# Optimization experiments

Hardware: AMD Instinct MI355X
Metric: run time of the kernel (lower is better)

Reference implementation:

```python
import jax, jax.numpy as jnp
import numpy as np

D_MODEL = 1024
HEADS = 16
DIM_HEAD = 64
INNER = HEADS * DIM_HEAD


def setup_inputs() -> dict:
    key = jax.random.key(0)
    ks = jax.random.split(key, 5)
    B, N = 4, 2048
    x = jax.random.normal(ks[0], (B, N, D_MODEL), dtype=jnp.float32)
    w_qkv = jax.random.normal(ks[1], (INNER * 3, D_MODEL), dtype=jnp.float32) * (1.0 / np.sqrt(D_MODEL))
    b_qkv = jax.random.normal(ks[2], (INNER * 3,), dtype=jnp.float32) * 0.02
    w_out = jax.random.normal(ks[3], (D_MODEL, INNER), dtype=jnp.float32) * (1.0 / np.sqrt(INNER))
    logit_scale = jnp.log(10.0 * jnp.ones((HEADS, 1, 1), dtype=jnp.float32))
    return {"x": x, "w_qkv": w_qkv, "b_qkv": b_qkv, "w_out": w_out, "logit_scale": logit_scale}


def _l2norm(t, eps=1e-12):
    # matches F.normalize(dim=-1): x / max(||x||, eps)
    n = jnp.sqrt(jnp.sum(t * t, axis=-1, keepdims=True))
    return t / jnp.maximum(n, eps)


def reference(x, w_qkv, b_qkv, w_out, logit_scale):
    B, N, C = x.shape
    qkv = x @ w_qkv.T + b_qkv                      # [B,N,3*INNER]
    qkv = qkv.reshape(B, N, 3, HEADS, DIM_HEAD)
    qkv = jnp.transpose(qkv, (2, 0, 3, 1, 4))       # [3,B,H,N,Dh]
    q, k, v = qkv[0], qkv[1], qkv[2]
    attn = jnp.einsum('bhnd,bhmd->bhnm', _l2norm(q), _l2norm(k))
    scale = jnp.exp(jnp.minimum(logit_scale, jnp.log(1.0 / 0.01)))  # [H,1,1]
    attn = attn * scale[None]                       # broadcast over batch
    attn = jax.nn.softmax(attn, axis=-1)
    out = jnp.einsum('bhnm,bhmd->bhnd', attn, v)    # [B,H,N,Dh]
    out = jnp.transpose(out, (0, 2, 1, 3)).reshape(B, N, C)
    return out @ w_out.T
```

## Files before the change

### kernel.cpp

```cpp
#include <hip/hip_runtime.h>

typedef __attribute__((ext_vector_type(8))) __bf16 bf16x8;
typedef __attribute__((ext_vector_type(4))) float f32x4;
typedef unsigned short u16;

__device__ __forceinline__ u16 f2bf(float f) {
    union { float f; unsigned u; } v; v.f = f;
    unsigned r = v.u + 0x7FFFu + ((v.u >> 16) & 1u);
    return (u16)(r >> 16);
}
__device__ __forceinline__ float bf2f(u16 h) {
    union { unsigned u; float f; } v; v.u = ((unsigned)h) << 16;
    return v.f;
}
__device__ __forceinline__ u16 f2bf_n(float f) {
    union { __bf16 b; u16 u; } t; t.b = (__bf16)f; return t.u;
}
__device__ __forceinline__ bf16x8 ld_bf16x8(const u16* p) {
    union { uint4 u; bf16x8 b; } t;
    t.u = *(const uint4*)p;
    return t.b;
}
__device__ __forceinline__ void async16(const void* g, const void* l) {
    __builtin_amdgcn_global_load_lds((const __attribute__((address_space(1))) void*)g,
                                     (__attribute__((address_space(3))) void*)l, 16, 0, 0);
}

#define BATCH 4
#define NSEQ 2048
#define HEADS 16
#define DH 64
#define DMODEL 1024
#define MROWS 8192
#define NQKV 3072

__global__ void split_bf16(const float* __restrict__ src, u16* __restrict__ hi,
                           u16* __restrict__ lo, int n) {
    int i = blockIdx.x * blockDim.x + threadIdx.x;
    if (i < n) {
        float f = src[i];
        u16 h = f2bf(f);
        hi[i] = h;
        lo[i] = f2bf(f - bf2f(h));
    }
}
__global__ void cvt_bf16(const float* __restrict__ src, u16* __restrict__ dst, int n) {
    int i = blockIdx.x * blockDim.x + threadIdx.x;
    if (i < n) dst[i] = f2bf(src[i]);
}

__global__ __launch_bounds__(256) void qkv_gemm(
    const u16* __restrict__ A,
    const u16* __restrict__ Bh, const u16* __restrict__ Bl,
    const float* __restrict__ bias,
    u16* __restrict__ Qn, u16* __restrict__ Kn, u16* __restrict__ Vt) {
    const int K = DMODEL, TK = 32;
    __shared__ __align__(16) u16 sA[128 * 32];
    __shared__ __align__(16) u16 sBh[128 * 32], sBl[128 * 32];
    const int tid = threadIdx.x, wave = tid >> 6, lane = tid & 63;
    const int quad = lane >> 4, l16 = lane & 15;
    const int m0 = blockIdx.x * 128, n0 = blockIdx.y * 128;
    const int wm = (wave & 1) * 64, wn = (wave >> 1) * 64;
    f32x4 acc[4][4] = {};

    for (int k0 = 0; k0 < K; k0 += TK) {
        __syncthreads();
        #pragma unroll
        for (int pass = 0; pass < 2; ++pass) {
            const int c = pass * 256 + tid;
            const int row = c >> 2, part = c & 3;
            const int ldsOff = (pass * 256 + wave * 64) * 16;
            const size_t ga = (size_t)(m0 + row) * K + k0 + part * 8;
            const size_t gb = (size_t)(n0 + row) * K + k0 + part * 8;
            async16(A + ga, (const char*)sA + ldsOff);
            async16(Bh + gb, (const char*)sBh + ldsOff);
            async16(Bl + gb, (const char*)sBl + ldsOff);
        }
        __syncthreads();
        bf16x8 a[4];
        #pragma unroll
        for (int mt = 0; mt < 4; ++mt)
            a[mt] = ld_bf16x8(&sA[(wm + mt * 16 + l16) * TK + quad * 8]);
        #pragma unroll
        for (int nt = 0; nt < 4; ++nt) {
            const int cix = wn + nt * 16 + l16;
            bf16x8 bh = ld_bf16x8(&sBh[cix * TK + quad * 8]);
            bf16x8 bl = ld_bf16x8(&sBl[cix * TK + quad * 8]);
            #pragma unroll
            for (int mt = 0; mt < 4; ++mt) {
                acc[mt][nt] = __builtin_amdgcn_mfma_f32_16x16x32_bf16(a[mt], bh, acc[mt][nt], 0, 0, 0);
                acc[mt][nt] = __builtin_amdgcn_mfma_f32_16x16x32_bf16(a[mt], bl, acc[mt][nt], 0, 0, 0);
            }
        }
    }

    #pragma unroll
    for (int nt = 0; nt < 4; ++nt) {
        const float bv = bias[n0 + wn + nt * 16 + l16];
        #pragma unroll
        for (int mt = 0; mt < 4; ++mt)
            #pragma unroll
            for (int r = 0; r < 4; ++r)
                acc[mt][nt][r] += bv;
    }

    if (n0 < 2048) {
        u16* dst = (n0 < 1024) ? Qn : Kn;
        const int nq = (n0 & 1023) + wn;
        const int hh = nq >> 6;
        #pragma unroll
        for (int mt = 0; mt < 4; ++mt) {
            float ss[4] = {};
            #pragma unroll
            for (int nt = 0; nt < 4; ++nt)
                #pragma unroll
                for (int r = 0; r < 4; ++r)
                    ss[r] += acc[mt][nt][r] * acc[mt][nt][r];
            #pragma unroll
            for (int r = 0; r < 4; ++r) {
                ss[r] += __shfl_xor(ss[r], 1);
                ss[r] += __shfl_xor(ss[r], 2);
                ss[r] += __shfl_xor(ss[r], 4);
                ss[r] += __shfl_xor(ss[r], 8);
                ss[r] = 1.f / fmaxf(sqrtf(ss[r]), 1e-12f);
            }
            const int mbase = m0 + wm + mt * 16 + quad * 4;
            const int b = mbase >> 11, n = mbase & 2047;
            #pragma unroll
            for (int r = 0; r < 4; ++r) {
                size_t rowoff = (((size_t)(b * HEADS + hh)) * NSEQ + n + r) * DH;
                #pragma unroll
                for (int nt = 0; nt < 4; ++nt)
                    dst[rowoff + nt * 16 + l16] = f2bf_n(acc[mt][nt][r] * ss[r]);
            }
        }
    } else {
        const int nv = (n0 - 2048) + wn;
        const int hh = nv >> 6;
        #pragma unroll
        for (int nt = 0; nt < 4; ++nt) {
            const int d = nt * 16 + l16;
            #pragma unroll
            for (int mt = 0; mt < 4; ++mt) {
                const int mbase = m0 + wm + mt * 16 + quad * 4;
                const int b = mbase >> 11, n = mbase & 2047;
                ushort4 t;
                t.x = f2bf_n(acc[mt][nt][0]);
                t.y = f2bf_n(acc[mt][nt][1]);
                t.z = f2bf_n(acc[mt][nt][2]);
                t.w = f2bf_n(acc[mt][nt][3]);
                *(ushort4*)&Vt[(((size_t)(b * HEADS + hh)) * DH + d) * NSEQ + n] = t;
            }
        }
    }
}

__global__ __launch_bounds__(256) void out_gemm(
    const u16* __restrict__ A, const u16* __restrict__ B, float* __restrict__ C) {
    const int K = DMODEL, N = DMODEL, TK = 32;
    __shared__ __align__(16) u16 sA[128 * 32], sB[128 * 32];
    const int tid = threadIdx.x, wave = tid >> 6, lane = tid & 63;
    const int quad = lane >> 4, l16 = lane & 15;
    const int m0 = blockIdx.x * 128, n0 = blockIdx.y * 128;
    const int wm = (wave & 1) * 64, wn = (wave >> 1) * 64;
    f32x4 acc[4][4] = {};

    for (int k0 = 0; k0 < K; k0 += TK) {
        __syncthreads();
        #pragma unroll
        for (int pass = 0; pass < 2; ++pass) {
            const int c = pass * 256 + tid;
            const int row = c >> 2, part = c & 3;
            const int ldsOff = (pass * 256 + wave * 64) * 16;
            const size_t ga = (size_t)(m0 + row) * K + k0 + part * 8;
            const size_t gb = (size_t)(n0 + row) * K + k0 + part * 8;
            async16(A + ga, (const char*)sA + ldsOff);
            async16(B + gb, (const char*)sB + ldsOff);
        }
        __syncthreads();
        bf16x8 a[4];
        #pragma unroll
        for (int mt = 0; mt < 4; ++mt)
            a[mt] = ld_bf16x8(&sA[(wm + mt * 16 + l16) * TK + quad * 8]);
        #pragma unroll
        for (int nt = 0; nt < 4; ++nt) {
            bf16x8 b = ld_bf16x8(&sB[(wn + nt * 16 + l16) * TK + quad * 8]);
            #pragma unroll
            for (int mt = 0; mt < 4; ++mt)
                acc[mt][nt] = __builtin_amdgcn_mfma_f32_16x16x32_bf16(a[mt], b, acc[mt][nt], 0, 0, 0);
        }
    }
    #pragma unroll
    for (int nt = 0; nt < 4; ++nt) {
        const int n = n0 + wn + nt * 16 + l16;
        #pragma unroll
        for (int mt = 0; mt < 4; ++mt) {
            const int mbase = m0 + wm + mt * 16 + quad * 4;
            #pragma unroll
            for (int r = 0; r < 4; ++r)
                C[(size_t)(mbase + r) * N + n] = acc[mt][nt][r];
        }
    }
}

__global__ __launch_bounds__(512) void flash_attn(
    const u16* __restrict__ Q, const u16* __restrict__ Kn, const u16* __restrict__ Vt,
    const float* __restrict__ lsc, u16* __restrict__ AO) {
    const int bh = blockIdx.x;
    const int q0 = blockIdx.y * 128;
    const int h = bh & (HEADS - 1), b = bh >> 4;
    const int tid = threadIdx.x, wave = tid >> 6, lane = tid & 63;
    const int quad = lane >> 4, l16 = lane & 15;
    const float scale = __expf(fminf(lsc[h], 4.6051702f));
    const float c1 = scale * 1.4426950408889634f;

    __shared__ __align__(16) u16 Ks[64][72];
    __shared__ __align__(16) u16 Vs[64][72];
    __shared__ __align__(16) u16 Ps[8][16][72];

    const u16* qbase = Q + ((size_t)bh * NSEQ + q0 + wave * 16) * DH;
    bf16x8 qa[2];
    qa[0] = ld_bf16x8(qbase + l16 * DH + quad * 8);
    qa[1] = ld_bf16x8(qbase + l16 * DH + 32 + quad * 8);

    f32x4 O[4] = {};
    float lr[4] = {0.f, 0.f, 0.f, 0.f};

    const int row = tid >> 3, part = tid & 7;
    const u16* kb = Kn + (size_t)bh * NSEQ * DH + (size_t)row * DH + part * 8;
    const u16* vb = Vt + (size_t)bh * DH * NSEQ + (size_t)row * NSEQ + part * 8;

    uint4 kA = *(const uint4*)kb;
    uint4 vA = *(const uint4*)vb;
    uint4 kB, vB;

    auto compute = [&]() {
        f32x4 S[4] = {};
        __builtin_amdgcn_s_setprio(1);
        #pragma unroll
        for (int nt = 0; nt < 4; ++nt) {
            bf16x8 k0 = ld_bf16x8(&Ks[nt * 16 + l16][quad * 8]);
            bf16x8 k1 = ld_bf16x8(&Ks[nt * 16 + l16][32 + quad * 8]);
            S[nt] = __builtin_amdgcn_mfma_f32_16x16x32_bf16(qa[0], k0, S[nt], 0, 0, 0);
            S[nt] = __builtin_amdgcn_mfma_f32_16x16x32_bf16(qa[1], k1, S[nt], 0, 0, 0);
        }
        __builtin_amdgcn_s_setprio(0);

        #pragma unroll
        for (int nt = 0; nt < 4; ++nt) {
            #pragma unroll
            for (int r = 0; r < 4; ++r) {
                float pv = __builtin_amdgcn_exp2f(__builtin_fmaf(S[nt][r], c1, -c1));
                lr[r] += pv;
                Ps[wave][quad * 4 + r][nt * 16 + l16] = f2bf_n(pv);
            }
        }
        asm volatile("s_waitcnt lgkmcnt(0)" ::: "memory");
        bf16x8 pa0 = ld_bf16x8(&Ps[wave][l16][quad * 8]);
        bf16x8 pa1 = ld_bf16x8(&Ps[wave][l16][32 + quad * 8]);

        __builtin_amdgcn_s_setprio(1);
        #pragma unroll
        for (int dt = 0; dt < 4; ++dt) {
            bf16x8 v0 = ld_bf16x8(&Vs[dt * 16 + l16][quad * 8]);
            bf16x8 v1 = ld_bf16x8(&Vs[dt * 16 + l16][32 + quad * 8]);
            O[dt] = __builtin_amdgcn_mfma_f32_16x16x32_bf16(pa0, v0, O[dt], 0, 0, 0);
            O[dt] = __builtin_amdgcn_mfma_f32_16x16x32_bf16(pa1, v1, O[dt], 0, 0, 0);
        }
        __builtin_amdgcn_s_setprio(0);
    };

    #pragma unroll 1
    for (int kt = 0; kt < NSEQ; kt += 128) {
        asm volatile("s_waitcnt lgkmcnt(0)" ::: "memory");
        __builtin_amdgcn_s_barrier();
        kB = *(const uint4*)(kb + (size_t)(kt + 64) * DH);
        vB = *(const uint4*)(vb + (kt + 64));
        asm volatile("s_waitcnt vmcnt(2)" ::: "memory");
        *(uint4*)&Ks[row][part * 8] = kA;
        *(uint4*)&Vs[row][part * 8] = vA;
        asm volatile("s_waitcnt lgkmcnt(0)" ::: "memory");
        __builtin_amdgcn_s_barrier();
        compute();

        asm volatile("s_waitcnt lgkmcnt(0)" ::: "memory");
        __builtin_amdgcn_s_barrier();
        {
            const int nk = (kt + 128) < NSEQ ? (kt + 128) : 0;
            kA = *(const uint4*)(kb + (size_t)nk * DH);
            vA = *(const uint4*)(vb + nk);
        }
        asm volatile("s_waitcnt vmcnt(2)" ::: "memory");
        *(uint4*)&Ks[row][part * 8] = kB;
        *(uint4*)&Vs[row][part * 8] = vB;
        asm volatile("s_waitcnt lgkmcnt(0)" ::: "memory");
        __builtin_amdgcn_s_barrier();
        compute();
    }

    #pragma unroll
    for (int r = 0; r < 4; ++r) {
        float s = lr[r];
        s += __shfl_xor(s, 1);
        s += __shfl_xor(s, 2);
        s += __shfl_xor(s, 4);
        s += __shfl_xor(s, 8);
        lr[r] = fmaxf(s, 1e-30f);
    }

    #pragma unroll
    for (int r = 0; r < 4; ++r) {
        float inv = 1.f / lr[r];
        size_t orow = (size_t)b * NSEQ + q0 + wave * 16 + quad * 4 + r;
        #pragma unroll
        for (int dt = 0; dt < 4; ++dt)
            AO[orow * DMODEL + h * DH + dt * 16 + l16] = f2bf_n(O[dt][r] * inv);
    }
}

extern "C" void kernel_launch(void* const* d_in, const int* in_sizes, int n_in,
                              void* d_out, int out_size, void* d_ws, size_t ws_size,
                              hipStream_t stream) {
    const float* x    = (const float*)d_in[0];
    const float* wqkv = (const float*)d_in[1];
    const float* bqkv = (const float*)d_in[2];
    const float* wout = (const float*)d_in[3];
    const float* lsc  = (const float*)d_in[4];

    char* ws = (char*)d_ws;
    u16* xb   = (u16*)(ws + 0);
    u16* wqh  = (u16*)(ws + 16777216);
    u16* wql  = (u16*)(ws + 23068672);
    u16* wob  = (u16*)(ws + 29360128);
    u16* qn   = (u16*)(ws + 31457280);
    u16* kn   = (u16*)(ws + 48234496);
    u16* vt   = (u16*)(ws + 65011712);
    u16* ao   = xb;

    cvt_bf16<<<MROWS * DMODEL / 256, 256, 0, stream>>>(x, xb, MROWS * DMODEL);
    split_bf16<<<NQKV * DMODEL / 256, 256, 0, stream>>>(wqkv, wqh, wql, NQKV * DMODEL);
    cvt_bf16<<<DMODEL * DMODEL / 256, 256, 0, stream>>>(wout, wob, DMODEL * DMODEL);

    qkv_gemm<<<dim3(MROWS / 128, NQKV / 128), 256, 0, stream>>>(xb, wqh, wql, bqkv, qn, kn, vt);
    flash_attn<<<dim3(BATCH * HEADS, NSEQ / 128), 512, 0, stream>>>(qn, kn, vt, lsc, ao);
    out_gemm<<<dim3(MROWS / 128, DMODEL / 128), 256, 0, stream>>>(ao, wob, (float*)d_out);
}
```

Before: 357.9 us.

## Triple-buffer QKV GEMM with swizzled LDS, larger tiles and 512 threads

Rewrites the QKV projection GEMM as a 3-stage async LDS pipeline over 64 K-steps, with hi and lo weight halves streamed as separate passes rather than interleaved per step. The block tile grows to 256x128 with 8 waves, LDS reads use an XOR swizzle to avoid bank conflicts, and MFMA sections run at raised priority. The aim is to hide global-load latency and drop one of the two barriers per step. In exchange it uses more LDS per block, and the output epilogue must still match the new wave-to-tile mapping.

```diff
diff --git a/kernel.cpp b/kernel.cpp
--- a/kernel.cpp
+++ b/kernel.cpp
@@ -49,50 +49,72 @@
     if (i < n) dst[i] = f2bf(src[i]);
 }
 
-__global__ __launch_bounds__(256) void qkv_gemm(
+#define QBUF 24576
+
+__global__ __launch_bounds__(512, 2) void qkv_gemm(
     const u16* __restrict__ A,
     const u16* __restrict__ Bh, const u16* __restrict__ Bl,
     const float* __restrict__ bias,
     u16* __restrict__ Qn, u16* __restrict__ Kn, u16* __restrict__ Vt) {
-    const int K = DMODEL, TK = 32;
-    __shared__ __align__(16) u16 sA[128 * 32];
-    __shared__ __align__(16) u16 sBh[128 * 32], sBl[128 * 32];
+    __shared__ __align__(1024) char lds[3 * QBUF];
     const int tid = threadIdx.x, wave = tid >> 6, lane = tid & 63;
     const int quad = lane >> 4, l16 = lane & 15;
-    const int m0 = blockIdx.x * 128, n0 = blockIdx.y * 128;
-    const int wm = (wave & 1) * 64, wn = (wave >> 1) * 64;
+    const int wr = wave >> 1, wc = wave & 1;
+    const int wm = wr * 64, wn = wc * 64;
+    const int m0 = blockIdx.x * 256, n0 = blockIdx.y * 128;
+
+    const int srow = tid >> 2;
+    const int sq = (tid & 3) ^ ((srow >> 1) & 3);
+    const char* aSrc0 = (const char*)A + (size_t)(m0 + srow) * 2048 + sq * 16;
+    const char* aSrc1 = aSrc0 + (size_t)128 * 2048;
+    const size_t bRow = (size_t)(n0 + srow) * 2048 + (size_t)(sq * 16);
+    const char* bSrcH = (const char*)Bh + bRow;
+    const char* bSrcL = (const char*)Bl + bRow;
+    const int ldsW = wave * 1024;
+
+    auto stage = [&](int src, int buf) {
+        const int kk = (src & 31) * 64;
+        const char* bs = (src < 32 ? bSrcH : bSrcL) + kk;
+        char* d = lds + buf * QBUF;
+        async16(aSrc0 + kk, d + ldsW);
+        async16(aSrc1 + kk, d + 8192 + ldsW);
+        async16(bs, d + 16384 + ldsW);
+    };
+
+    const int rq = (quad ^ ((l16 >> 1) & 3)) * 16;
+
     f32x4 acc[4][4] = {};
 
-    for (int k0 = 0; k0 < K; k0 += TK) {
-        __syncthreads();
-        #pragma unroll
-        for (int pass = 0; pass < 2; ++pass) {
-            const int c = pass * 256 + tid;
-            const int row = c >> 2, part = c & 3;
-            const int ldsOff = (pass * 256 + wave * 64) * 16;
-            const size_t ga = (size_t)(m0 + row) * K + k0 + part * 8;
-            const size_t gb = (size_t)(n0 + row) * K + k0 + part * 8;
-            async16(A + ga, (const char*)sA + ldsOff);
-            async16(Bh + gb, (const char*)sBh + ldsOff);
-            async16(Bl + gb, (const char*)sBl + ldsOff);
-        }
-        __syncthreads();
-        bf16x8 a[4];
+    stage(0, 0);
+    stage(1, 1);
+
+    int bufc = 0, bufs = 2;
+    #pragma unroll 1
+    for (int t = 0; t < 64; ++t) {
+        asm volatile("s_waitcnt vmcnt(3)" ::: "memory");
+        __builtin_amdgcn_s_barrier();
+        __builtin_amdgcn_sched_barrier(0);
+        stage((t + 2) & 63, bufs);
+        const char* bufA = lds + bufc * QBUF;
+        const char* bufB = bufA + 16384;
+        bf16x8 af[4], bfr[4];
         #pragma unroll
         for (int mt = 0; mt < 4; ++mt)
-            a[mt] = ld_bf16x8(&sA[(wm + mt * 16 + l16) * TK + quad * 8]);
-        #pragma unroll
-        for (int nt = 0; nt < 4; ++nt) {
-            const int cix = wn + nt * 16 + l16;
-            bf16x8 bh = ld_bf16x8(&sBh[cix * TK + quad * 8]);
-            bf16x8 bl = ld_bf16x8(&sBl[cix * TK + quad * 8]);
-            #pragma unroll
-            for (int mt = 0; mt < 4; ++mt) {
-                acc[mt][nt] = __builtin_amdgcn_mfma_f32_16x16x32_bf16(a[mt], bh, acc[mt][nt], 0, 0, 0);
-                acc[mt][nt] = __builtin_amdgcn_mfma_f32_16x16x32_bf16(a[mt], bl, acc[mt][nt], 0, 0, 0);
-            }
-        }
-    }
+            af[mt] = ld_bf16x8((const u16*)(bufA + (wm + mt * 16 + l16) * 64 + rq));
+        #pragma unroll
+        for (int nt = 0; nt < 4; ++nt)
+            bfr[nt] = ld_bf16x8((const u16*)(bufB + (wn + nt * 16 + l16) * 64 + rq));
+        __builtin_amdgcn_s_setprio(1);
+        #pragma unroll
+        for (int nt = 0; nt < 4; ++nt)
+            #pragma unroll
+            for (int mt = 0; mt < 4; ++mt)
+                acc[mt][nt] = __builtin_amdgcn_mfma_f32_16x16x32_bf16(af[mt], bfr[nt], acc[mt][nt], 0, 0, 0);
+        __builtin_amdgcn_s_setprio(0);
+        bufc = (bufc == 2) ? 0 : bufc + 1;
+        bufs = (bufs == 2) ? 0 : bufs + 1;
+    }
+    asm volatile("s_waitcnt vmcnt(0)" ::: "memory");
 
     #pragma unroll
     for (int nt = 0; nt < 4; ++nt) {
@@ -341,7 +363,7 @@
     split_bf16<<<NQKV * DMODEL / 256, 256, 0, stream>>>(wqkv, wqh, wql, NQKV * DMODEL);
     cvt_bf16<<<DMODEL * DMODEL / 256, 256, 0, stream>>>(wout, wob, DMODEL * DMODEL);
 
-    qkv_gemm<<<dim3(MROWS / 128, NQKV / 128), 256, 0, stream>>>(xb, wqh, wql, bqkv, qn, kn, vt);
+    qkv_gemm<<<dim3(MROWS / 256, NQKV / 128), 512, 0, stream>>>(xb, wqh, wql, bqkv, qn, kn, vt);
     flash_attn<<<dim3(BATCH * HEADS, NSEQ / 128), 512, 0, stream>>>(qn, kn, vt, lsc, ao);
     out_gemm<<<dim3(MROWS / 128, DMODEL / 128), 256, 0, stream>>>(ao, wob, (float*)d_out);
 }
```

Result: slower. 382.0 us (+6.8%).

## Rewrite QKV GEMM as 256x256 tiled, double-buffered, swizzled-LDS pipelined kernel

Applied to the files above, without the earlier changes.

Replaces the 128x128 QKV GEMM with a 256x256 tile over 8 waves. It double-buffers 64 KB LDS stages with XOR-swizzled layouts and interleaves async global-to-LDS loads with MFMA phases, using explicit barriers, vmcnt waits and s_setprio. The bf16 hi/lo weight halves are now concatenated along K (32 k-steps) rather than issuing two MFMAs per A fragment. The aim is to hide load latency, cut LDS bank conflicts and raise data reuse per tile, at the cost of heavier register pressure and lower occupancy, plus fragile hand-managed synchronization.

```diff
diff --git a/kernel.cpp b/kernel.cpp
--- a/kernel.cpp
+++ b/kernel.cpp
@@ -49,73 +49,129 @@
     if (i < n) dst[i] = f2bf(src[i]);
 }
 
-__global__ __launch_bounds__(256) void qkv_gemm(
+#define QK_BUF 65536
+
+#define QBAR() asm volatile("s_barrier" ::: "memory")
+
+#define RD_AF(QH, BB) { \
+    _Pragma("unroll") for (int mi = 0; mi < 4; ++mi) { \
+        const int rr = wm + (QH) * 64 + mi * 16 + l16; \
+        af[mi][0] = ld_bf16x8((const u16*)(lds + (BB) + rr * 128 + qsw0)); \
+        af[mi][1] = ld_bf16x8((const u16*)(lds + (BB) + rr * 128 + qsw1)); } }
+
+#define RD_BF(DST, NB, BB) { \
+    _Pragma("unroll") for (int ni = 0; ni < 2; ++ni) { \
+        const int rr = wn + (NB) * 32 + ni * 16 + l16; \
+        DST[ni][0] = ld_bf16x8((const u16*)(lds + (BB) + 32768 + rr * 128 + qsw0)); \
+        DST[ni][1] = ld_bf16x8((const u16*)(lds + (BB) + 32768 + rr * 128 + qsw1)); } }
+
+#define ST_A(KT, H, BB) { \
+    const char* g = aRow + (size_t)(H) * 262144 + (((KT) & 15) << 7); \
+    char* d = lds + (BB) + (H) * 16384 + wave * 1024; \
+    async16(g, d); async16(g + 131072, d + 8192); }
+
+#define ST_B(KT, H, BB) { \
+    const char* g = (((KT) < 16) ? bhRow : blRow) + (size_t)(H) * 262144 + (((KT) & 15) << 7); \
+    char* d = lds + (BB) + 32768 + (H) * 16384 + wave * 1024; \
+    async16(g, d); async16(g + 131072, d + 8192); }
+
+#define MFMA_Q(MIB, NIB) { \
+    __builtin_amdgcn_s_setprio(1); \
+    _Pragma("unroll") for (int ks = 0; ks < 2; ++ks) \
+    _Pragma("unroll") for (int mi = 0; mi < 4; ++mi) \
+    _Pragma("unroll") for (int ni = 0; ni < 2; ++ni) \
+        acc[(MIB) + mi][(NIB) + ni] = __builtin_amdgcn_mfma_f32_16x16x32_bf16( \
+            af[mi][ks], ((NIB) ? b1 : b0)[ni][ks], acc[(MIB) + mi][(NIB) + ni], 0, 0, 0); \
+    __builtin_amdgcn_s_setprio(0); }
+
+__global__ __launch_bounds__(512, 2) void qkv_gemm(
     const u16* __restrict__ A,
     const u16* __restrict__ Bh, const u16* __restrict__ Bl,
     const float* __restrict__ bias,
     u16* __restrict__ Qn, u16* __restrict__ Kn, u16* __restrict__ Vt) {
-    const int K = DMODEL, TK = 32;
-    __shared__ __align__(16) u16 sA[128 * 32];
-    __shared__ __align__(16) u16 sBh[128 * 32], sBl[128 * 32];
+    __shared__ __align__(1024) char lds[2 * QK_BUF];
     const int tid = threadIdx.x, wave = tid >> 6, lane = tid & 63;
     const int quad = lane >> 4, l16 = lane & 15;
-    const int m0 = blockIdx.x * 128, n0 = blockIdx.y * 128;
-    const int wm = (wave & 1) * 64, wn = (wave >> 1) * 64;
-    f32x4 acc[4][4] = {};
-
-    for (int k0 = 0; k0 < K; k0 += TK) {
-        __syncthreads();
-        #pragma unroll
-        for (int pass = 0; pass < 2; ++pass) {
-            const int c = pass * 256 + tid;
-            const int row = c >> 2, part = c & 3;
-            const int ldsOff = (pass * 256 + wave * 64) * 16;
-            const size_t ga = (size_t)(m0 + row) * K + k0 + part * 8;
-            const size_t gb = (size_t)(n0 + row) * K + k0 + part * 8;
-            async16(A + ga, (const char*)sA + ldsOff);
-            async16(Bh + gb, (const char*)sBh + ldsOff);
-            async16(Bl + gb, (const char*)sBl + ldsOff);
-        }
-        __syncthreads();
-        bf16x8 a[4];
-        #pragma unroll
-        for (int mt = 0; mt < 4; ++mt)
-            a[mt] = ld_bf16x8(&sA[(wm + mt * 16 + l16) * TK + quad * 8]);
-        #pragma unroll
-        for (int nt = 0; nt < 4; ++nt) {
-            const int cix = wn + nt * 16 + l16;
-            bf16x8 bh = ld_bf16x8(&sBh[cix * TK + quad * 8]);
-            bf16x8 bl = ld_bf16x8(&sBl[cix * TK + quad * 8]);
-            #pragma unroll
-            for (int mt = 0; mt < 4; ++mt) {
-                acc[mt][nt] = __builtin_amdgcn_mfma_f32_16x16x32_bf16(a[mt], bh, acc[mt][nt], 0, 0, 0);
-                acc[mt][nt] = __builtin_amdgcn_mfma_f32_16x16x32_bf16(a[mt], bl, acc[mt][nt], 0, 0, 0);
-            }
-        }
-    }
+    const int wm = (wave >> 2) * 128, wn = (wave & 3) * 64;
+    const int m0 = blockIdx.x * 256, n0 = blockIdx.y * 256;
+
+    const int lr0 = tid >> 3;
+    const int qs = ((tid & 7) ^ (lr0 & 7)) * 16;
+    const char* aRow  = (const char*)A  + (size_t)(m0 + lr0) * 2048 + qs;
+    const char* bhRow = (const char*)Bh + (size_t)(n0 + lr0) * 2048 + qs;
+    const char* blRow = (const char*)Bl + (size_t)(n0 + lr0) * 2048 + qs;
+
+    const int qsw0 = ((0 * 4 + quad) ^ (l16 & 7)) * 16;
+    const int qsw1 = ((1 * 4 + quad) ^ (l16 & 7)) * 16;
+
+    f32x4 acc[8][4] = {};
+    bf16x8 af[4][2], b0[2][2], b1[2][2];
+
+    ST_A(0, 0, 0); ST_A(0, 1, 0); ST_B(0, 0, 0); ST_B(0, 1, 0);
+    ST_A(1, 0, QK_BUF); ST_A(1, 1, QK_BUF); ST_B(1, 0, QK_BUF); ST_B(1, 1, QK_BUF);
+    asm volatile("s_waitcnt vmcnt(8)" ::: "memory");
+    QBAR();
+
+    #pragma unroll 1
+    for (int t = 0; t < 16; ++t) {
+        const int k1 = 2 * t + 1;
+        const int k2 = (2 * t + 2) & 31;
+        const int k3 = (2 * t + 3) & 31;
+        RD_AF(0, 0); RD_BF(b0, 0, 0);
+        ST_A(k1, 1, QK_BUF);
+        QBAR(); MFMA_Q(0, 0); QBAR();
+
+        RD_BF(b1, 1, 0);
+        ST_B(k1, 0, QK_BUF);
+        QBAR(); MFMA_Q(0, 2); QBAR();
+
+        RD_AF(1, 0);
+        ST_B(k1, 1, QK_BUF);
+        QBAR(); MFMA_Q(4, 0); QBAR();
+
+        ST_A(k2, 0, 0);
+        asm volatile("s_waitcnt vmcnt(2)" ::: "memory");
+        QBAR(); MFMA_Q(4, 2); QBAR();
+        RD_AF(0, QK_BUF); RD_BF(b0, 0, QK_BUF);
+        ST_A(k2, 1, 0);
+        QBAR(); MFMA_Q(0, 0); QBAR();
+
+        RD_BF(b1, 1, QK_BUF);
+        ST_B(k2, 0, 0);
+        QBAR(); MFMA_Q(0, 2); QBAR();
+
+        RD_AF(1, QK_BUF);
+        ST_B(k2, 1, 0);
+        QBAR(); MFMA_Q(4, 0); QBAR();
+
+        ST_A(k3, 0, QK_BUF);
+        asm volatile("s_waitcnt vmcnt(2)" ::: "memory");
+        QBAR(); MFMA_Q(4, 2); QBAR();
+    }
+    asm volatile("s_waitcnt vmcnt(0)" ::: "memory");
+    QBAR();
 
     #pragma unroll
-    for (int nt = 0; nt < 4; ++nt) {
-        const float bv = bias[n0 + wn + nt * 16 + l16];
-        #pragma unroll
-        for (int mt = 0; mt < 4; ++mt)
+    for (int ni = 0; ni < 4; ++ni) {
+        const float bv = bias[n0 + wn + ni * 16 + l16];
+        #pragma unroll
+        for (int mi = 0; mi < 8; ++mi)
             #pragma unroll
             for (int r = 0; r < 4; ++r)
-                acc[mt][nt][r] += bv;
+                acc[mi][ni][r] += bv;
     }
 
     if (n0 < 2048) {
         u16* dst = (n0 < 1024) ? Qn : Kn;
-        const int nq = (n0 & 1023) + wn;
-        const int hh = nq >> 6;
-        #pragma unroll
-        for (int mt = 0; mt < 4; ++mt) {
+        const int hh = ((n0 & 1023) + wn) >> 6;
+        #pragma unroll
+        for (int mi = 0; mi < 8; ++mi) {
             float ss[4] = {};
             #pragma unroll
-            for (int nt = 0; nt < 4; ++nt)
+            for (int ni = 0; ni < 4; ++ni)
                 #pragma unroll
                 for (int r = 0; r < 4; ++r)
-                    ss[r] += acc[mt][nt][r] * acc[mt][nt][r];
+                    ss[r] += acc[mi][ni][r] * acc[mi][ni][r];
             #pragma unroll
             for (int r = 0; r < 4; ++r) {
                 ss[r] += __shfl_xor(ss[r], 1);
@@ -124,31 +180,30 @@
                 ss[r] += __shfl_xor(ss[r], 8);
                 ss[r] = 1.f / fmaxf(sqrtf(ss[r]), 1e-12f);
             }
-            const int mbase = m0 + wm + mt * 16 + quad * 4;
+            const int mbase = m0 + wm + mi * 16 + quad * 4;
             const int b = mbase >> 11, n = mbase & 2047;
             #pragma unroll
             for (int r = 0; r < 4; ++r) {
                 size_t rowoff = (((size_t)(b * HEADS + hh)) * NSEQ + n + r) * DH;
                 #pragma unroll
-                for (int nt = 0; nt < 4; ++nt)
-                    dst[rowoff + nt * 16 + l16] = f2bf_n(acc[mt][nt][r] * ss[r]);
+                for (int ni = 0; ni < 4; ++ni)
+                    dst[rowoff + ni * 16 + l16] = f2bf_n(acc[mi][ni][r] * ss[r]);
             }
         }
     } else {
-        const int nv = (n0 - 2048) + wn;
-        const int hh = nv >> 6;
-        #pragma unroll
-        for (int nt = 0; nt < 4; ++nt) {
-            const int d = nt * 16 + l16;
-            #pragma unroll
-            for (int mt = 0; mt < 4; ++mt) {
-                const int mbase = m0 + wm + mt * 16 + quad * 4;
+        const int hh = ((n0 - 2048) + wn) >> 6;
+        #pragma unroll
+        for (int ni = 0; ni < 4; ++ni) {
+            const int d = ni * 16 + l16;
+            #pragma unroll
+            for (int mi = 0; mi < 8; ++mi) {
+                const int mbase = m0 + wm + mi * 16 + quad * 4;
                 const int b = mbase >> 11, n = mbase & 2047;
                 ushort4 t;
-                t.x = f2bf_n(acc[mt][nt][0]);
-                t.y = f2bf_n(acc[mt][nt][1]);
-                t.z = f2bf_n(acc[mt][nt][2]);
-                t.w = f2bf_n(acc[mt][nt][3]);
+                t.x = f2bf_n(acc[mi][ni][0]);
+                t.y = f2bf_n(acc[mi][ni][1]);
+                t.z = f2bf_n(acc[mi][ni][2]);
+                t.w = f2bf_n(acc[mi][ni][3]);
                 *(ushort4*)&Vt[(((size_t)(b * HEADS + hh)) * DH + d) * NSEQ + n] = t;
             }
         }
@@ -341,7 +396,7 @@
     split_bf16<<<NQKV * DMODEL / 256, 256, 0, stream>>>(wqkv, wqh, wql, NQKV * DMODEL);
     cvt_bf16<<<DMODEL * DMODEL / 256, 256, 0, stream>>>(wout, wob, DMODEL * DMODEL);
 
-    qkv_gemm<<<dim3(MROWS / 128, NQKV / 128), 256, 0, stream>>>(xb, wqh, wql, bqkv, qn, kn, vt);
+    qkv_gemm<<<dim3(MROWS / 256, NQKV / 256), 512, 0, stream>>>(xb, wqh, wql, bqkv, qn, kn, vt);
     flash_attn<<<dim3(BATCH * HEADS, NSEQ / 128), 512, 0, stream>>>(qn, kn, vt, lsc, ao);
     out_gemm<<<dim3(MROWS / 128, DMODEL / 128), 256, 0, stream>>>(ao, wob, (float*)d_out);
 }
```

Result: slower. 416.2 us (+16.3%).

## Fuse conversion kernels and keep attention probabilities in registers via transposed MFMA

Applied to the files above, without the earlier changes.

Merges the three fp32-to-bf16 conversion launches into one vectorized prep kernel, cutting launch overhead and widening memory accesses. In flash attention, the QK^T MFMA operands are swapped so each lane holds score columns. The probabilities are then packed to bf16 with v_cvt_pk_bf16_f32 and redistributed with lane shuffles instead of a round trip through a shared-memory P buffer. Row sums become one per-lane accumulator reduced at the end, at the cost of extra shuffle instructions.

```diff
diff --git a/kernel.cpp b/kernel.cpp
--- a/kernel.cpp
+++ b/kernel.cpp
@@ -33,20 +33,34 @@
 #define DMODEL 1024
 #define MROWS 8192
 #define NQKV 3072
-
-__global__ void split_bf16(const float* __restrict__ src, u16* __restrict__ hi,
-                           u16* __restrict__ lo, int n) {
-    int i = blockIdx.x * blockDim.x + threadIdx.x;
-    if (i < n) {
-        float f = src[i];
-        u16 h = f2bf(f);
-        hi[i] = h;
-        lo[i] = f2bf(f - bf2f(h));
-    }
-}
-__global__ void cvt_bf16(const float* __restrict__ src, u16* __restrict__ dst, int n) {
-    int i = blockIdx.x * blockDim.x + threadIdx.x;
-    if (i < n) dst[i] = f2bf(src[i]);
+#define XE 8388608
+#define WE 3145728
+#define OE 1048576
+
+__global__ __launch_bounds__(256) void prep(
+    const float* __restrict__ x, const float* __restrict__ wqkv,
+    const float* __restrict__ wout,
+    u16* __restrict__ xb, u16* __restrict__ wqh, u16* __restrict__ wql,
+    u16* __restrict__ wob) {
+    const int i4 = (blockIdx.x * 256 + threadIdx.x) * 4;
+    if (i4 < XE) {
+        float4 v = *(const float4*)(x + i4);
+        ushort4 t = { f2bf(v.x), f2bf(v.y), f2bf(v.z), f2bf(v.w) };
+        *(ushort4*)(xb + i4) = t;
+    } else if (i4 < XE + WE) {
+        const int j = i4 - XE;
+        float4 v = *(const float4*)(wqkv + j);
+        ushort4 h = { f2bf(v.x), f2bf(v.y), f2bf(v.z), f2bf(v.w) };
+        ushort4 l = { f2bf(v.x - bf2f(h.x)), f2bf(v.y - bf2f(h.y)),
+                      f2bf(v.z - bf2f(h.z)), f2bf(v.w - bf2f(h.w)) };
+        *(ushort4*)(wqh + j) = h;
+        *(ushort4*)(wql + j) = l;
+    } else {
+        const int j = i4 - XE - WE;
+        float4 v = *(const float4*)(wout + j);
+        ushort4 t = { f2bf(v.x), f2bf(v.y), f2bf(v.z), f2bf(v.w) };
+        *(ushort4*)(wob + j) = t;
+    }
 }
 
 __global__ __launch_bounds__(256) void qkv_gemm(
@@ -216,7 +230,6 @@
 
     __shared__ __align__(16) u16 Ks[64][72];
     __shared__ __align__(16) u16 Vs[64][72];
-    __shared__ __align__(16) u16 Ps[8][16][72];
 
     const u16* qbase = Q + ((size_t)bh * NSEQ + q0 + wave * 16) * DH;
     bf16x8 qa[2];
@@ -224,7 +237,7 @@
     qa[1] = ld_bf16x8(qbase + l16 * DH + 32 + quad * 8);
 
     f32x4 O[4] = {};
-    float lr[4] = {0.f, 0.f, 0.f, 0.f};
+    float lrs = 0.f;
 
     const int row = tid >> 3, part = tid & 7;
     const u16* kb = Kn + (size_t)bh * NSEQ * DH + (size_t)row * DH + part * 8;
@@ -241,31 +254,43 @@
         for (int nt = 0; nt < 4; ++nt) {
             bf16x8 k0 = ld_bf16x8(&Ks[nt * 16 + l16][quad * 8]);
             bf16x8 k1 = ld_bf16x8(&Ks[nt * 16 + l16][32 + quad * 8]);
-            S[nt] = __builtin_amdgcn_mfma_f32_16x16x32_bf16(qa[0], k0, S[nt], 0, 0, 0);
-            S[nt] = __builtin_amdgcn_mfma_f32_16x16x32_bf16(qa[1], k1, S[nt], 0, 0, 0);
+            S[nt] = __builtin_amdgcn_mfma_f32_16x16x32_bf16(k0, qa[0], S[nt], 0, 0, 0);
+            S[nt] = __builtin_amdgcn_mfma_f32_16x16x32_bf16(k1, qa[1], S[nt], 0, 0, 0);
         }
         __builtin_amdgcn_s_setprio(0);
 
-        #pragma unroll
-        for (int nt = 0; nt < 4; ++nt) {
-            #pragma unroll
-            for (int r = 0; r < 4; ++r) {
-                float pv = __builtin_amdgcn_exp2f(__builtin_fmaf(S[nt][r], c1, -c1));
-                lr[r] += pv;
-                Ps[wave][quad * 4 + r][nt * 16 + l16] = f2bf_n(pv);
-            }
-        }
-        asm volatile("s_waitcnt lgkmcnt(0)" ::: "memory");
-        bf16x8 pa0 = ld_bf16x8(&Ps[wave][l16][quad * 8]);
-        bf16x8 pa1 = ld_bf16x8(&Ps[wave][l16][32 + quad * 8]);
+        unsigned w[4][2];
+        #pragma unroll
+        for (int nt = 0; nt < 4; ++nt) {
+            #pragma unroll
+            for (int p = 0; p < 2; ++p) {
+                float a = __builtin_amdgcn_exp2f(__builtin_fmaf(S[nt][2 * p], c1, -c1));
+                float c = __builtin_amdgcn_exp2f(__builtin_fmaf(S[nt][2 * p + 1], c1, -c1));
+                lrs += a + c;
+                asm("v_cvt_pk_bf16_f32 %0, %1, %2" : "=v"(w[nt][p]) : "v"(a), "v"(c));
+            }
+        }
+        bf16x8 pf[2];
+        #pragma unroll
+        for (int kc = 0; kc < 2; ++kc) {
+            union { unsigned u[4]; bf16x8 b; } t;
+            #pragma unroll
+            for (int j = 0; j < 4; ++j) {
+                const int src = l16 + (2 * (quad & 1) + (j >> 1)) * 16;
+                unsigned lo = (unsigned)__shfl((int)w[2 * kc][j & 1], src);
+                unsigned hi = (unsigned)__shfl((int)w[2 * kc + 1][j & 1], src);
+                t.u[j] = (quad & 2) ? hi : lo;
+            }
+            pf[kc] = t.b;
+        }
 
         __builtin_amdgcn_s_setprio(1);
         #pragma unroll
         for (int dt = 0; dt < 4; ++dt) {
             bf16x8 v0 = ld_bf16x8(&Vs[dt * 16 + l16][quad * 8]);
             bf16x8 v1 = ld_bf16x8(&Vs[dt * 16 + l16][32 + quad * 8]);
-            O[dt] = __builtin_amdgcn_mfma_f32_16x16x32_bf16(pa0, v0, O[dt], 0, 0, 0);
-            O[dt] = __builtin_amdgcn_mfma_f32_16x16x32_bf16(pa1, v1, O[dt], 0, 0, 0);
+            O[dt] = __builtin_amdgcn_mfma_f32_16x16x32_bf16(pf[0], v0, O[dt], 0, 0, 0);
+            O[dt] = __builtin_amdgcn_mfma_f32_16x16x32_bf16(pf[1], v1, O[dt], 0, 0, 0);
         }
         __builtin_amdgcn_s_setprio(0);
     };
@@ -298,19 +323,13 @@
         compute();
     }
 
+    lrs += __shfl_xor(lrs, 16);
+    lrs += __shfl_xor(lrs, 32);
+
     #pragma unroll
     for (int r = 0; r < 4; ++r) {
-        float s = lr[r];
-        s += __shfl_xor(s, 1);
-        s += __shfl_xor(s, 2);
-        s += __shfl_xor(s, 4);
-        s += __shfl_xor(s, 8);
-        lr[r] = fmaxf(s, 1e-30f);
-    }
-
-    #pragma unroll
-    for (int r = 0; r < 4; ++r) {
-        float inv = 1.f / lr[r];
+        const float lq = __shfl(lrs, quad * 4 + r);
+        const float inv = 1.f / fmaxf(lq, 1e-30f);
         size_t orow = (size_t)b * NSEQ + q0 + wave * 16 + quad * 4 + r;
         #pragma unroll
         for (int dt = 0; dt < 4; ++dt)
@@ -337,9 +356,7 @@
     u16* vt   = (u16*)(ws + 65011712);
     u16* ao   = xb;
 
-    cvt_bf16<<<MROWS * DMODEL / 256, 256, 0, stream>>>(x, xb, MROWS * DMODEL);
-    split_bf16<<<NQKV * DMODEL / 256, 256, 0, stream>>>(wqkv, wqh, wql, NQKV * DMODEL);
-    cvt_bf16<<<DMODEL * DMODEL / 256, 256, 0, stream>>>(wout, wob, DMODEL * DMODEL);
+    prep<<<(XE + WE + OE) / 1024, 256, 0, stream>>>(x, wqkv, wout, xb, wqh, wql, wob);
 
     qkv_gemm<<<dim3(MROWS / 128, NQKV / 128), 256, 0, stream>>>(xb, wqh, wql, bqkv, qn, kn, vt);
     flash_attn<<<dim3(BATCH * HEADS, NSEQ / 128), 512, 0, stream>>>(qn, kn, vt, lsc, ao);
```

Measured after the change: 358.6 us. Within noise of the previous version (+0.2%).
